# Optimization experiments

Hardware: AMD Instinct MI355X
Metric: run time of the kernel (lower is better)

Reference implementation:

```python
import jax, jax.numpy as jnp
import numpy as np

N_NODES = 100000


def _mean_agg(x, src, dst, n_nodes):
    # gather neighbor (src) features, segment-sum into destination nodes, divide by in-degree
    summed = jax.ops.segment_sum(x[src], dst, num_segments=n_nodes)  # [N, d]
    deg = jax.ops.segment_sum(jnp.ones_like(dst, dtype=x.dtype), dst, num_segments=n_nodes)
    return summed / jnp.clip(deg, 1.0)[:, None]  # DGL clamps zero in-degree to 1


def _sage_conv(x, src, dst, W_self, W_neigh, b, n_nodes):
    h_neigh = _mean_agg(x, src, dst, n_nodes)
    # DGL SAGEConv(mean): fc_self(h_self) + fc_neigh(h_neigh); single bias
    return x @ W_self + h_neigh @ W_neigh + b


def setup_inputs() -> dict:
    key = jax.random.key(0)
    ks = jax.random.split(key, 8)
    in_f, hid_f, out_f = 64, 64, 16
    n_edges = 1200000
    return {
        "x": jax.random.normal(ks[0], (N_NODES, in_f), dtype=jnp.float32),
        "src": jax.random.randint(ks[1], (n_edges,), 0, N_NODES),
        "dst": jax.random.randint(ks[2], (n_edges,), 0, N_NODES),
        "W1_self": jax.random.normal(ks[3], (in_f, hid_f), dtype=jnp.float32) / np.sqrt(in_f),
        "W1_neigh": jax.random.normal(ks[4], (in_f, hid_f), dtype=jnp.float32) / np.sqrt(in_f),
        "b1": jnp.zeros((hid_f,), dtype=jnp.float32),
        "W2_self": jax.random.normal(ks[5], (hid_f, out_f), dtype=jnp.float32) / np.sqrt(hid_f),
        "W2_neigh": jax.random.normal(ks[6], (hid_f, out_f), dtype=jnp.float32) / np.sqrt(hid_f),
        "b2": jnp.zeros((out_f,), dtype=jnp.float32),
    }


def reference(x, src, dst, W1_self, W1_neigh, b1, W2_self, W2_neigh, b2):
    h = _sage_conv(x, src, dst, W1_self, W1_neigh, b1, N_NODES)
    h = jax.nn.relu(h)
    h = _sage_conv(h, src, dst, W2_self, W2_neigh, b2, N_NODES)
    return h
```

## Files before the change

kernel.cpp:

```cpp
#include <hip/hip_runtime.h>

#define N_NODES 100000
#define N_EDGES 1200000
#define BK 128
#define NB 782
#define CHUNK_E 4096
#define NBLK_E 293
#define TOT_H (NB * NBLK_E)
#define NSB2 ((TOT_H + 1023) / 1024)
#define CAP 4096
#define ND1 3125

#define OFF_ROWPTR 0
#define OFF_HISTG  400896
#define OFF_HSCAN  1317632
#define OFF_BLK2   2234368
#define OFF_PAIRS  2235392
#define OFF_SORTED 7035392
#define OFF_Y1     11835392
#define OFF_H1     24635392

__device__ __forceinline__ unsigned short f2bf(float f) {
    unsigned u = __float_as_uint(f);
    unsigned r = (u + 0x7fffu + ((u >> 16) & 1u)) >> 16;
    return (unsigned short)r;
}

__global__ __launch_bounds__(256) void hist_dense1_kernel(
    const int* __restrict__ dst, int* __restrict__ hist_g,
    const float* __restrict__ x,
    const float* __restrict__ Wn, const float* __restrict__ Ws,
    const float* __restrict__ b,
    unsigned short* __restrict__ y1, float* __restrict__ z1)
{
    __shared__ float sx[32 * 64];
    const int t = threadIdx.x;

    if (blockIdx.x < NBLK_E) {
        int* h = (int*)sx;
        const int e0 = blockIdx.x * CHUNK_E;
        const int e1 = min(e0 + CHUNK_E, N_EDGES);
        for (int i = t; i < NB; i += 256) h[i] = 0;
        __syncthreads();
        for (int e = e0 + t; e < e1; e += 256)
            atomicAdd(&h[dst[e] >> 7], 1);
        __syncthreads();
        for (int i = t; i < NB; i += 256)
            hist_g[i * NBLK_E + blockIdx.x] = h[i];
        return;
    }

    const int bid = blockIdx.x - NBLK_E;
    const int w = t >> 6;
    const int lane = t & 63;
    const int half = w >> 1;
    const int nsub = (w & 1) * 16;
    const int chunk = bid * 32;

    {
        const float4* gx = (const float4*)(x + (size_t)chunk * 64);
        float4* sx4 = (float4*)sx;
        sx4[t] = gx[t];
        sx4[t + 256] = gx[t + 256];
    }

    const float* W = half ? Ws : Wn;
    float wr[64];
#pragma unroll
    for (int k = 0; k < 64; ++k) wr[k] = W[k * 64 + lane];
    const float bj = half ? b[lane] : 0.f;

    __syncthreads();

#pragma unroll 1
    for (int m = 0; m < 16; ++m) {
        const int node = nsub + m;
        const float4* xr = (const float4*)(sx + node * 64);
        float a0 = 0.f, a1 = 0.f, a2 = 0.f, a3 = 0.f;
#pragma unroll
        for (int k4 = 0; k4 < 16; ++k4) {
            float4 v = xr[k4];
            a0 += v.x * wr[4 * k4 + 0];
            a1 += v.y * wr[4 * k4 + 1];
            a2 += v.z * wr[4 * k4 + 2];
            a3 += v.w * wr[4 * k4 + 3];
        }
        const float o = (a0 + a1) + (a2 + a3) + bj;
        const size_t gn = (size_t)(chunk + node);
        if (half) z1[gn * 64 + lane] = o;
        else      y1[gn * 64 + lane] = f2bf(o);
    }
}

__global__ __launch_bounds__(1024) void scan2_blocks_kernel(
    const int* __restrict__ hist_g, int* __restrict__ hs_scan, int* __restrict__ blk2)
{
    __shared__ int s[1024];
    int i = blockIdx.x * 1024 + threadIdx.x;
    int v = (i < TOT_H) ? hist_g[i] : 0;
    s[threadIdx.x] = v;
    __syncthreads();
    for (int off = 1; off < 1024; off <<= 1) {
        int t = (threadIdx.x >= off) ? s[threadIdx.x - off] : 0;
        __syncthreads();
        s[threadIdx.x] += t;
        __syncthreads();
    }
    if (i < TOT_H) hs_scan[i] = s[threadIdx.x] - v;
    if (threadIdx.x == 1023) blk2[blockIdx.x] = s[1023];
}

__device__ __forceinline__ void local_tops_scan(const int* blk2, int* tops, int t)
{
    if (t < 256) {
        int v = (t < NSB2) ? blk2[t] : 0;
        tops[t] = v;
    }
    __syncthreads();
    for (int off = 1; off < 256; off <<= 1) {
        int tv = (t >= off && t < 256) ? tops[t - off] : 0;
        __syncthreads();
        if (t < 256) tops[t] += tv;
        __syncthreads();
    }
    int ex = 0;
    if (t < 256) ex = tops[t] - ((t < NSB2) ? blk2[t] : 0);
    __syncthreads();
    if (t < 256) tops[t] = ex;
    __syncthreads();
}

__global__ __launch_bounds__(256) void pair_scatter_kernel(
    const int* __restrict__ src, const int* __restrict__ dst,
    const int* __restrict__ hs_scan, const int* __restrict__ blk2,
    unsigned* __restrict__ pairs)
{
    __shared__ int base_s[NB];
    __shared__ int cur_s[NB];
    __shared__ int tops[256];
    const int b = blockIdx.x;
    const int t = threadIdx.x;
    const int e0 = b * CHUNK_E;
    const int e1 = min(e0 + CHUNK_E, N_EDGES);

    local_tops_scan(blk2, tops, t);

    for (int i = t; i < NB; i += 256) {
        int idx = i * NBLK_E + b;
        base_s[i] = hs_scan[idx] + tops[idx >> 10];
        cur_s[i] = 0;
    }
    __syncthreads();
    for (int e = e0 + t; e < e1; e += 256) {
        int d = dst[e];
        int bk = d >> 7;
        int pos = base_s[bk] + atomicAdd(&cur_s[bk], 1);
        pairs[pos] = ((unsigned)src[e] << 7) | (unsigned)(d & 127);
    }
}

__global__ __launch_bounds__(512) void fused_gather1_kernel(
    const unsigned short* __restrict__ y1,
    const unsigned* __restrict__ pairs,
    const int* __restrict__ hs_scan, const int* __restrict__ blk2,
    int* __restrict__ row_ptr, int* __restrict__ sorted_src,
    float* __restrict__ h1)
{
    __shared__ int slist[CAP];
    __shared__ int hist[BK];
    __shared__ int sc[BK];
    __shared__ int cur[BK];
    __shared__ int tops[256];
    const int b = blockIdx.x;
    const int t = threadIdx.x;
    const int lane = t & 63;
    const int wv = t >> 6;
    const int g = lane >> 3;
    const int fl = lane & 7;

    local_tops_scan(blk2, tops, t);

    const int i0 = b * NBLK_E;
    const int start = hs_scan[i0] + tops[i0 >> 10];
    const int end = (b == NB - 1) ? N_EDGES
                    : hs_scan[i0 + NBLK_E] + tops[(i0 + NBLK_E) >> 10];
    const int cnt = end - start;
    const int node0 = b * BK;

    if (t < BK) hist[t] = 0;
    __syncthreads();
    for (int e = start + t; e < end; e += 512)
        atomicAdd(&hist[pairs[e] & 127u], 1);
    __syncthreads();

    int v = (t < BK) ? hist[t] : 0;
    if (t < BK) sc[t] = v;
    __syncthreads();
    for (int off = 1; off < BK; off <<= 1) {
        int tv = (t >= off && t < BK) ? sc[t - off] : 0;
        __syncthreads();
        if (t < BK) sc[t] += tv;
        __syncthreads();
    }
    const int excl = (t < BK) ? sc[t] - v : 0;
    if (t < BK && node0 + t < N_NODES) row_ptr[node0 + t] = start + excl;
    if (b == NB - 1 && t == 0) row_ptr[N_NODES] = N_EDGES;
    if (t < BK) cur[t] = excl;
    __syncthreads();

    if (cnt <= CAP) {
        for (int e = start + t; e < end; e += 512) {
            unsigned u = pairs[e];
            int p = atomicAdd(&cur[u & 127u], 1);
            slist[p] = (int)(u >> 7);
        }
        __syncthreads();
        for (int i = t; i < cnt; i += 512)
            sorted_src[start + i] = slist[i];
        for (int m = 0; m < 16; ++m) {
            const int node = wv * 16 + m;
            const int gn = node0 + node;
            if (gn >= N_NODES) break;
            const int o = sc[node] - hist[node];
            const int dg = hist[node];
            float a0 = 0.f, a1 = 0.f, a2 = 0.f, a3 = 0.f;
            float a4 = 0.f, a5 = 0.f, a6 = 0.f, a7 = 0.f;
            for (int base = 0; base < dg; base += 8) {
                const int idx = base + g;
                if (idx < dg) {
                    const int s = slist[o + idx];
                    uint4 raw = ((const uint4*)(y1 + (size_t)s * 64))[fl];
                    a0 += __uint_as_float(raw.x << 16);
                    a1 += __uint_as_float(raw.x & 0xffff0000u);
                    a2 += __uint_as_float(raw.y << 16);
                    a3 += __uint_as_float(raw.y & 0xffff0000u);
                    a4 += __uint_as_float(raw.z << 16);
                    a5 += __uint_as_float(raw.z & 0xffff0000u);
                    a6 += __uint_as_float(raw.w << 16);
                    a7 += __uint_as_float(raw.w & 0xffff0000u);
                }
            }
#pragma unroll
            for (int d = 8; d <= 32; d <<= 1) {
                a0 += __shfl_xor(a0, d); a1 += __shfl_xor(a1, d);
                a2 += __shfl_xor(a2, d); a3 += __shfl_xor(a3, d);
                a4 += __shfl_xor(a4, d); a5 += __shfl_xor(a5, d);
                a6 += __shfl_xor(a6, d); a7 += __shfl_xor(a7, d);
            }
            const float invd = 1.0f / (float)max(dg, 1);
            if (g == 0) {
                float4* hp = (float4*)(h1 + (size_t)gn * 64);
                float4 z0 = hp[fl * 2];
                float4 z1v = hp[fl * 2 + 1];
                hp[fl * 2] = make_float4(fmaxf(z0.x + a0 * invd, 0.f),
                                         fmaxf(z0.y + a1 * invd, 0.f),
                                         fmaxf(z0.z + a2 * invd, 0.f),
                                         fmaxf(z0.w + a3 * invd, 0.f));
                hp[fl * 2 + 1] = make_float4(fmaxf(z1v.x + a4 * invd, 0.f),
                                             fmaxf(z1v.y + a5 * invd, 0.f),
                                             fmaxf(z1v.z + a6 * invd, 0.f),
                                             fmaxf(z1v.w + a7 * invd, 0.f));
            }
        }
    } else {
        if (t < BK) cur[t] = start + excl;
        __syncthreads();
        for (int e = start + t; e < end; e += 512) {
            unsigned u = pairs[e];
            int p = atomicAdd(&cur[u & 127u], 1);
            sorted_src[p] = (int)(u >> 7);
        }
        __syncthreads();
        for (int m = 0; m < 16; ++m) {
            const int node = wv * 16 + m;
            const int gn = node0 + node;
            if (gn >= N_NODES) break;
            const int o = start + sc[node] - hist[node];
            const int dg = hist[node];
            float a0 = 0.f, a1 = 0.f, a2 = 0.f, a3 = 0.f;
            float a4 = 0.f, a5 = 0.f, a6 = 0.f, a7 = 0.f;
            for (int base = 0; base < dg; base += 8) {
                const int idx = base + g;
                if (idx < dg) {
                    const int s = sorted_src[o + idx];
                    uint4 raw = ((const uint4*)(y1 + (size_t)s * 64))[fl];
                    a0 += __uint_as_float(raw.x << 16);
                    a1 += __uint_as_float(raw.x & 0xffff0000u);
                    a2 += __uint_as_float(raw.y << 16);
                    a3 += __uint_as_float(raw.y & 0xffff0000u);
                    a4 += __uint_as_float(raw.z << 16);
                    a5 += __uint_as_float(raw.z & 0xffff0000u);
                    a6 += __uint_as_float(raw.w << 16);
                    a7 += __uint_as_float(raw.w & 0xffff0000u);
                }
            }
#pragma unroll
            for (int d = 8; d <= 32; d <<= 1) {
                a0 += __shfl_xor(a0, d); a1 += __shfl_xor(a1, d);
                a2 += __shfl_xor(a2, d); a3 += __shfl_xor(a3, d);
                a4 += __shfl_xor(a4, d); a5 += __shfl_xor(a5, d);
                a6 += __shfl_xor(a6, d); a7 += __shfl_xor(a7, d);
            }
            const float invd = 1.0f / (float)max(dg, 1);
            if (g == 0) {
                float4* hp = (float4*)(h1 + (size_t)gn * 64);
                float4 z0 = hp[fl * 2];
                float4 z1v = hp[fl * 2 + 1];
                hp[fl * 2] = make_float4(fmaxf(z0.x + a0 * invd, 0.f),
                                         fmaxf(z0.y + a1 * invd, 0.f),
                                         fmaxf(z0.z + a2 * invd, 0.f),
                                         fmaxf(z0.w + a3 * invd, 0.f));
                hp[fl * 2 + 1] = make_float4(fmaxf(z1v.x + a4 * invd, 0.f),
                                             fmaxf(z1v.y + a5 * invd, 0.f),
                                             fmaxf(z1v.z + a6 * invd, 0.f),
                                             fmaxf(z1v.w + a7 * invd, 0.f));
            }
        }
    }
}

__global__ __launch_bounds__(256) void dense2_kernel(
    const float* __restrict__ h1,
    const float* __restrict__ Wn, const float* __restrict__ Ws,
    const float* __restrict__ b,
    float* __restrict__ y2, float* __restrict__ out)
{
    __shared__ float sx[32 * 68];
    const int t = threadIdx.x;
    const int w = t >> 6;
    const int lane = t & 63;
    const int half = w >> 1;
    const int nsub = (w & 1) * 16;
    const int j = lane & 15;
    const int g = lane >> 4;
    const int chunk = blockIdx.x * 32;

    {
        const float4* gx = (const float4*)(h1 + (size_t)chunk * 64);
        float4* sx4 = (float4*)sx;
        int r0 = t >> 4, c0 = t & 15;
        sx4[r0 * 17 + c0] = gx[t];
        sx4[(r0 + 16) * 17 + c0] = gx[t + 256];
    }

    const float* W = half ? Ws : Wn;
    float wr[64];
#pragma unroll
    for (int k = 0; k < 64; ++k) wr[k] = W[k * 16 + j];
    const float bj = half ? b[j] : 0.f;

    __syncthreads();

#pragma unroll 1
    for (int q = 0; q < 4; ++q) {
        const int node = nsub + q * 4 + g;
        const float4* xr = (const float4*)(sx + node * 68);
        float a0 = 0.f, a1 = 0.f, a2 = 0.f, a3 = 0.f;
#pragma unroll
        for (int k4 = 0; k4 < 16; ++k4) {
            float4 v = xr[k4];
            a0 += v.x * wr[4 * k4 + 0];
            a1 += v.y * wr[4 * k4 + 1];
            a2 += v.z * wr[4 * k4 + 2];
            a3 += v.w * wr[4 * k4 + 3];
        }
        const float o = (a0 + a1) + (a2 + a3) + bj;
        const size_t gn = (size_t)(chunk + node);
        if (half) out[gn * 16 + j] = o;
        else      y2[gn * 16 + j] = o;
    }
}

__global__ __launch_bounds__(256) void gather2_kernel(
    const float* __restrict__ y2,
    const int* __restrict__ row_ptr,
    const int* __restrict__ sorted_src,
    float* __restrict__ out)
{
    const int wv = threadIdx.x >> 6;
    const int lane = threadIdx.x & 63;
    const int sub = lane >> 4;
    const int sl = lane & 15;
    const int eg = sl >> 2;
    const int fl = sl & 3;

    const int n = blockIdx.x * 16 + wv * 4 + sub;
    const int start = row_ptr[n];
    const int deg = row_ptr[n + 1] - start;

    float4 acc = make_float4(0.f, 0.f, 0.f, 0.f);
    for (int base = 0; base < deg; base += 16) {
        int eid = 0;
        if (base + sl < deg) eid = sorted_src[start + base + sl];
#pragma unroll
        for (int jj = 0; jj < 16; jj += 4) {
            const int idx = jj + eg;
            const int s = __shfl(eid, sub * 16 + idx);
            if (base + idx < deg) {
                float4 v = ((const float4*)(y2 + (size_t)s * 16))[fl];
                acc.x += v.x; acc.y += v.y; acc.z += v.z; acc.w += v.w;
            }
        }
    }
#pragma unroll
    for (int d = 4; d <= 8; d <<= 1) {
        acc.x += __shfl_xor(acc.x, d); acc.y += __shfl_xor(acc.y, d);
        acc.z += __shfl_xor(acc.z, d); acc.w += __shfl_xor(acc.w, d);
    }
    const float invd = 1.0f / (float)max(deg, 1);
    if (eg == 0) {
        float4* op = (float4*)(out + (size_t)n * 16);
        float4 z = op[fl];
        op[fl] = make_float4(z.x + acc.x * invd, z.y + acc.y * invd,
                             z.z + acc.z * invd, z.w + acc.w * invd);
    }
}

extern "C" void kernel_launch(void* const* d_in, const int* in_sizes, int n_in,
                              void* d_out, int out_size, void* d_ws, size_t ws_size,
                              hipStream_t stream) {
    const float* x   = (const float*)d_in[0];
    const int*   src = (const int*)d_in[1];
    const int*   dst = (const int*)d_in[2];
    const float* W1s = (const float*)d_in[3];
    const float* W1n = (const float*)d_in[4];
    const float* b1  = (const float*)d_in[5];
    const float* W2s = (const float*)d_in[6];
    const float* W2n = (const float*)d_in[7];
    const float* b2  = (const float*)d_in[8];
    float* out = (float*)d_out;

    char* ws = (char*)d_ws;
    int* row_ptr    = (int*)(ws + OFF_ROWPTR);
    int* hist_g     = (int*)(ws + OFF_HISTG);
    int* hs_scan    = (int*)(ws + OFF_HSCAN);
    int* blk2       = (int*)(ws + OFF_BLK2);
    unsigned* pairs = (unsigned*)(ws + OFF_PAIRS);
    int* sorted_src = (int*)(ws + OFF_SORTED);
    unsigned short* y1 = (unsigned short*)(ws + OFF_Y1);
    float* y2       = (float*)(ws + OFF_Y1);
    float* h1       = (float*)(ws + OFF_H1);

    hist_dense1_kernel<<<NBLK_E + ND1, 256, 0, stream>>>(
        dst, hist_g, x, W1n, W1s, b1, y1, h1);
    scan2_blocks_kernel<<<NSB2, 1024, 0, stream>>>(hist_g, hs_scan, blk2);
    pair_scatter_kernel<<<NBLK_E, 256, 0, stream>>>(src, dst, hs_scan, blk2, pairs);
    fused_gather1_kernel<<<NB, 512, 0, stream>>>(y1, pairs, hs_scan, blk2,
                                                 row_ptr, sorted_src, h1);
    dense2_kernel<<<ND1, 256, 0, stream>>>(h1, W2n, W2s, b2, y2, out);
    gather2_kernel<<<N_NODES / 16, 256, 0, stream>>>(y2, row_ptr, sorted_src, out);
}
```

Before: 226.7 us.

## Halve bucket size, rework gather1 lane mapping, scan histogram in place

Bucket width drops from 128 to 64 nodes, which doubles the number of gather1 blocks to 1563 and shrinks the shared slist capacity. Gather1 now has each wave handle two nodes at once, with 32 lanes per node and two neighbour loads in flight per iteration. The h1 and out residual values are loaded before the gather loop so their latency overlaps it. The histogram scan is written back into hist_g rather than a separate hs_scan buffer, and the tops scan and pair scatter move to 512 threads. The cost is a larger histogram to scan, more blocks that spill to the global-memory fallback path, and more shuffle and index overhead per node.

```diff
diff --git a/kernel.cpp b/kernel.cpp
--- a/kernel.cpp
+++ b/kernel.cpp
@@ -2,23 +2,22 @@
 
 #define N_NODES 100000
 #define N_EDGES 1200000
-#define BK 128
-#define NB 782
+#define BK 64
+#define NB 1563
 #define CHUNK_E 4096
 #define NBLK_E 293
 #define TOT_H (NB * NBLK_E)
 #define NSB2 ((TOT_H + 1023) / 1024)
-#define CAP 4096
+#define CAP 1536
 #define ND1 3125
 
 #define OFF_ROWPTR 0
-#define OFF_HISTG  400896
-#define OFF_HSCAN  1317632
+#define OFF_HISTG  401408
 #define OFF_BLK2   2234368
-#define OFF_PAIRS  2235392
-#define OFF_SORTED 7035392
-#define OFF_Y1     11835392
-#define OFF_H1     24635392
+#define OFF_PAIRS  2236416
+#define OFF_SORTED 7036928
+#define OFF_Y1     11837440
+#define OFF_H1     24637440
 
 __device__ __forceinline__ unsigned short f2bf(float f) {
     unsigned u = __float_as_uint(f);
@@ -43,7 +42,7 @@
         for (int i = t; i < NB; i += 256) h[i] = 0;
         __syncthreads();
         for (int e = e0 + t; e < e1; e += 256)
-            atomicAdd(&h[dst[e] >> 7], 1);
+            atomicAdd(&h[dst[e] >> 6], 1);
         __syncthreads();
         for (int i = t; i < NB; i += 256)
             hist_g[i * NBLK_E + blockIdx.x] = h[i];
@@ -93,7 +92,7 @@
 }
 
 __global__ __launch_bounds__(1024) void scan2_blocks_kernel(
-    const int* __restrict__ hist_g, int* __restrict__ hs_scan, int* __restrict__ blk2)
+    int* __restrict__ hist_g, int* __restrict__ blk2)
 {
     __shared__ int s[1024];
     int i = blockIdx.x * 1024 + threadIdx.x;
@@ -101,43 +100,40 @@
     s[threadIdx.x] = v;
     __syncthreads();
     for (int off = 1; off < 1024; off <<= 1) {
-        int t = (threadIdx.x >= off) ? s[threadIdx.x - off] : 0;
-        __syncthreads();
-        s[threadIdx.x] += t;
-        __syncthreads();
-    }
-    if (i < TOT_H) hs_scan[i] = s[threadIdx.x] - v;
+        int tv = (threadIdx.x >= off) ? s[threadIdx.x - off] : 0;
+        __syncthreads();
+        s[threadIdx.x] += tv;
+        __syncthreads();
+    }
+    if (i < TOT_H) hist_g[i] = s[threadIdx.x] - v;
     if (threadIdx.x == 1023) blk2[blockIdx.x] = s[1023];
 }
 
 __device__ __forceinline__ void local_tops_scan(const int* blk2, int* tops, int t)
 {
-    if (t < 256) {
-        int v = (t < NSB2) ? blk2[t] : 0;
-        tops[t] = v;
-    }
-    __syncthreads();
-    for (int off = 1; off < 256; off <<= 1) {
-        int tv = (t >= off && t < 256) ? tops[t - off] : 0;
-        __syncthreads();
-        if (t < 256) tops[t] += tv;
-        __syncthreads();
-    }
-    int ex = 0;
-    if (t < 256) ex = tops[t] - ((t < NSB2) ? blk2[t] : 0);
-    __syncthreads();
-    if (t < 256) tops[t] = ex;
-    __syncthreads();
-}
-
-__global__ __launch_bounds__(256) void pair_scatter_kernel(
+    int v = (t < NSB2) ? blk2[t] : 0;
+    tops[t] = v;
+    __syncthreads();
+    for (int off = 1; off < 512; off <<= 1) {
+        int tv = (t >= off) ? tops[t - off] : 0;
+        __syncthreads();
+        tops[t] += tv;
+        __syncthreads();
+    }
+    int ex = tops[t] - v;
+    __syncthreads();
+    tops[t] = ex;
+    __syncthreads();
+}
+
+__global__ __launch_bounds__(512) void pair_scatter_kernel(
     const int* __restrict__ src, const int* __restrict__ dst,
     const int* __restrict__ hs_scan, const int* __restrict__ blk2,
     unsigned* __restrict__ pairs)
 {
     __shared__ int base_s[NB];
     __shared__ int cur_s[NB];
-    __shared__ int tops[256];
+    __shared__ int tops[512];
     const int b = blockIdx.x;
     const int t = threadIdx.x;
     const int e0 = b * CHUNK_E;
@@ -145,17 +141,17 @@
 
     local_tops_scan(blk2, tops, t);
 
-    for (int i = t; i < NB; i += 256) {
+    for (int i = t; i < NB; i += 512) {
         int idx = i * NBLK_E + b;
         base_s[i] = hs_scan[idx] + tops[idx >> 10];
         cur_s[i] = 0;
     }
     __syncthreads();
-    for (int e = e0 + t; e < e1; e += 256) {
+    for (int e = e0 + t; e < e1; e += 512) {
         int d = dst[e];
-        int bk = d >> 7;
+        int bk = d >> 6;
         int pos = base_s[bk] + atomicAdd(&cur_s[bk], 1);
-        pairs[pos] = ((unsigned)src[e] << 7) | (unsigned)(d & 127);
+        pairs[pos] = ((unsigned)src[e] << 6) | (unsigned)(d & 63);
     }
 }
 
@@ -170,13 +166,9 @@
     __shared__ int hist[BK];
     __shared__ int sc[BK];
     __shared__ int cur[BK];
-    __shared__ int tops[256];
+    __shared__ int tops[512];
     const int b = blockIdx.x;
     const int t = threadIdx.x;
-    const int lane = t & 63;
-    const int wv = t >> 6;
-    const int g = lane >> 3;
-    const int fl = lane & 7;
 
     local_tops_scan(blk2, tops, t);
 
@@ -190,7 +182,7 @@
     if (t < BK) hist[t] = 0;
     __syncthreads();
     for (int e = start + t; e < end; e += 512)
-        atomicAdd(&hist[pairs[e] & 127u], 1);
+        atomicAdd(&hist[pairs[e] & 63u], 1);
     __syncthreads();
 
     int v = (t < BK) ? hist[t] : 0;
@@ -208,58 +200,85 @@
     if (t < BK) cur[t] = excl;
     __syncthreads();
 
+    const int wv = t >> 6;
+    const int lane = t & 63;
+    const int sub = lane >> 5;
+    const int sl = lane & 31;
+    const int eg = sl >> 3;
+    const int fl = sl & 7;
+
     if (cnt <= CAP) {
         for (int e = start + t; e < end; e += 512) {
             unsigned u = pairs[e];
-            int p = atomicAdd(&cur[u & 127u], 1);
-            slist[p] = (int)(u >> 7);
+            int p = atomicAdd(&cur[u & 63u], 1);
+            slist[p] = (int)(u >> 6);
         }
         __syncthreads();
         for (int i = t; i < cnt; i += 512)
             sorted_src[start + i] = slist[i];
-        for (int m = 0; m < 16; ++m) {
-            const int node = wv * 16 + m;
+        for (int q = 0; q < 4; ++q) {
+            const int node = wv * 8 + q * 2 + sub;
             const int gn = node0 + node;
             if (gn >= N_NODES) break;
             const int o = sc[node] - hist[node];
             const int dg = hist[node];
+            float4* hp = (float4*)(h1 + (size_t)gn * 64);
+            float4 z;
+            if (eg < 2) z = hp[fl * 2 + eg];
             float a0 = 0.f, a1 = 0.f, a2 = 0.f, a3 = 0.f;
             float a4 = 0.f, a5 = 0.f, a6 = 0.f, a7 = 0.f;
             for (int base = 0; base < dg; base += 8) {
-                const int idx = base + g;
-                if (idx < dg) {
-                    const int s = slist[o + idx];
-                    uint4 raw = ((const uint4*)(y1 + (size_t)s * 64))[fl];
-                    a0 += __uint_as_float(raw.x << 16);
-                    a1 += __uint_as_float(raw.x & 0xffff0000u);
-                    a2 += __uint_as_float(raw.y << 16);
-                    a3 += __uint_as_float(raw.y & 0xffff0000u);
-                    a4 += __uint_as_float(raw.z << 16);
-                    a5 += __uint_as_float(raw.z & 0xffff0000u);
-                    a6 += __uint_as_float(raw.w << 16);
-                    a7 += __uint_as_float(raw.w & 0xffff0000u);
+                const int i0e = base + eg;
+                const int i1e = base + 4 + eg;
+                const bool v0 = i0e < dg, v1 = i1e < dg;
+                uint4 r0, r1;
+                if (v0) {
+                    const int s = slist[o + i0e];
+                    r0 = ((const uint4*)(y1 + (size_t)s * 64))[fl];
                 }
-            }
-#pragma unroll
-            for (int d = 8; d <= 32; d <<= 1) {
+                if (v1) {
+                    const int s = slist[o + i1e];
+                    r1 = ((const uint4*)(y1 + (size_t)s * 64))[fl];
+                }
+                if (v0) {
+                    a0 += __uint_as_float(r0.x << 16);
+                    a1 += __uint_as_float(r0.x & 0xffff0000u);
+                    a2 += __uint_as_float(r0.y << 16);
+                    a3 += __uint_as_float(r0.y & 0xffff0000u);
+                    a4 += __uint_as_float(r0.z << 16);
+                    a5 += __uint_as_float(r0.z & 0xffff0000u);
+                    a6 += __uint_as_float(r0.w << 16);
+                    a7 += __uint_as_float(r0.w & 0xffff0000u);
+                }
+                if (v1) {
+                    a0 += __uint_as_float(r1.x << 16);
+                    a1 += __uint_as_float(r1.x & 0xffff0000u);
+                    a2 += __uint_as_float(r1.y << 16);
+                    a3 += __uint_as_float(r1.y & 0xffff0000u);
+                    a4 += __uint_as_float(r1.z << 16);
+                    a5 += __uint_as_float(r1.z & 0xffff0000u);
+                    a6 += __uint_as_float(r1.w << 16);
+                    a7 += __uint_as_float(r1.w & 0xffff0000u);
+                }
+            }
+#pragma unroll
+            for (int d = 8; d <= 16; d <<= 1) {
                 a0 += __shfl_xor(a0, d); a1 += __shfl_xor(a1, d);
                 a2 += __shfl_xor(a2, d); a3 += __shfl_xor(a3, d);
                 a4 += __shfl_xor(a4, d); a5 += __shfl_xor(a5, d);
                 a6 += __shfl_xor(a6, d); a7 += __shfl_xor(a7, d);
             }
             const float invd = 1.0f / (float)max(dg, 1);
-            if (g == 0) {
-                float4* hp = (float4*)(h1 + (size_t)gn * 64);
-                float4 z0 = hp[fl * 2];
-                float4 z1v = hp[fl * 2 + 1];
-                hp[fl * 2] = make_float4(fmaxf(z0.x + a0 * invd, 0.f),
-                                         fmaxf(z0.y + a1 * invd, 0.f),
-                                         fmaxf(z0.z + a2 * invd, 0.f),
-                                         fmaxf(z0.w + a3 * invd, 0.f));
-                hp[fl * 2 + 1] = make_float4(fmaxf(z1v.x + a4 * invd, 0.f),
-                                             fmaxf(z1v.y + a5 * invd, 0.f),
-                                             fmaxf(z1v.z + a6 * invd, 0.f),
-                                             fmaxf(z1v.w + a7 * invd, 0.f));
+            if (eg == 0) {
+                hp[fl * 2] = make_float4(fmaxf(z.x + a0 * invd, 0.f),
+                                         fmaxf(z.y + a1 * invd, 0.f),
+                                         fmaxf(z.z + a2 * invd, 0.f),
+                                         fmaxf(z.w + a3 * invd, 0.f));
+            } else if (eg == 1) {
+                hp[fl * 2 + 1] = make_float4(fmaxf(z.x + a4 * invd, 0.f),
+                                             fmaxf(z.y + a5 * invd, 0.f),
+                                             fmaxf(z.z + a6 * invd, 0.f),
+                                             fmaxf(z.w + a7 * invd, 0.f));
             }
         }
     } else {
@@ -267,20 +286,23 @@
         __syncthreads();
         for (int e = start + t; e < end; e += 512) {
             unsigned u = pairs[e];
-            int p = atomicAdd(&cur[u & 127u], 1);
-            sorted_src[p] = (int)(u >> 7);
-        }
-        __syncthreads();
-        for (int m = 0; m < 16; ++m) {
-            const int node = wv * 16 + m;
+            int p = atomicAdd(&cur[u & 63u], 1);
+            sorted_src[p] = (int)(u >> 6);
+        }
+        __syncthreads();
+        for (int q = 0; q < 4; ++q) {
+            const int node = wv * 8 + q * 2 + sub;
             const int gn = node0 + node;
             if (gn >= N_NODES) break;
             const int o = start + sc[node] - hist[node];
             const int dg = hist[node];
+            float4* hp = (float4*)(h1 + (size_t)gn * 64);
+            float4 z;
+            if (eg < 2) z = hp[fl * 2 + eg];
             float a0 = 0.f, a1 = 0.f, a2 = 0.f, a3 = 0.f;
             float a4 = 0.f, a5 = 0.f, a6 = 0.f, a7 = 0.f;
-            for (int base = 0; base < dg; base += 8) {
-                const int idx = base + g;
+            for (int base = 0; base < dg; base += 4) {
+                const int idx = base + eg;
                 if (idx < dg) {
                     const int s = sorted_src[o + idx];
                     uint4 raw = ((const uint4*)(y1 + (size_t)s * 64))[fl];
@@ -295,25 +317,23 @@
                 }
             }
 #pragma unroll
-            for (int d = 8; d <= 32; d <<= 1) {
+            for (int d = 8; d <= 16; d <<= 1) {
                 a0 += __shfl_xor(a0, d); a1 += __shfl_xor(a1, d);
                 a2 += __shfl_xor(a2, d); a3 += __shfl_xor(a3, d);
                 a4 += __shfl_xor(a4, d); a5 += __shfl_xor(a5, d);
                 a6 += __shfl_xor(a6, d); a7 += __shfl_xor(a7, d);
             }
             const float invd = 1.0f / (float)max(dg, 1);
-            if (g == 0) {
-                float4* hp = (float4*)(h1 + (size_t)gn * 64);
-                float4 z0 = hp[fl * 2];
-                float4 z1v = hp[fl * 2 + 1];
-                hp[fl * 2] = make_float4(fmaxf(z0.x + a0 * invd, 0.f),
-                                         fmaxf(z0.y + a1 * invd, 0.f),
-                                         fmaxf(z0.z + a2 * invd, 0.f),
-                                         fmaxf(z0.w + a3 * invd, 0.f));
-                hp[fl * 2 + 1] = make_float4(fmaxf(z1v.x + a4 * invd, 0.f),
-                                             fmaxf(z1v.y + a5 * invd, 0.f),
-                                             fmaxf(z1v.z + a6 * invd, 0.f),
-                                             fmaxf(z1v.w + a7 * invd, 0.f));
+            if (eg == 0) {
+                hp[fl * 2] = make_float4(fmaxf(z.x + a0 * invd, 0.f),
+                                         fmaxf(z.y + a1 * invd, 0.f),
+                                         fmaxf(z.z + a2 * invd, 0.f),
+                                         fmaxf(z.w + a3 * invd, 0.f));
+            } else if (eg == 1) {
+                hp[fl * 2 + 1] = make_float4(fmaxf(z.x + a4 * invd, 0.f),
+                                             fmaxf(z.y + a5 * invd, 0.f),
+                                             fmaxf(z.z + a6 * invd, 0.f),
+                                             fmaxf(z.w + a7 * invd, 0.f));
             }
         }
     }
@@ -388,6 +408,10 @@
     const int start = row_ptr[n];
     const int deg = row_ptr[n + 1] - start;
 
+    float4* op = (float4*)(out + (size_t)n * 16);
+    float4 z;
+    if (eg == 0) z = op[fl];
+
     float4 acc = make_float4(0.f, 0.f, 0.f, 0.f);
     for (int base = 0; base < deg; base += 16) {
         int eid = 0;
@@ -409,8 +433,6 @@
     }
     const float invd = 1.0f / (float)max(deg, 1);
     if (eg == 0) {
-        float4* op = (float4*)(out + (size_t)n * 16);
-        float4 z = op[fl];
         op[fl] = make_float4(z.x + acc.x * invd, z.y + acc.y * invd,
                              z.z + acc.z * invd, z.w + acc.w * invd);
     }
@@ -433,7 +455,6 @@
     char* ws = (char*)d_ws;
     int* row_ptr    = (int*)(ws + OFF_ROWPTR);
     int* hist_g     = (int*)(ws + OFF_HISTG);
-    int* hs_scan    = (int*)(ws + OFF_HSCAN);
     int* blk2       = (int*)(ws + OFF_BLK2);
     unsigned* pairs = (unsigned*)(ws + OFF_PAIRS);
     int* sorted_src = (int*)(ws + OFF_SORTED);
@@ -443,9 +464,9 @@
 
     hist_dense1_kernel<<<NBLK_E + ND1, 256, 0, stream>>>(
         dst, hist_g, x, W1n, W1s, b1, y1, h1);
-    scan2_blocks_kernel<<<NSB2, 1024, 0, stream>>>(hist_g, hs_scan, blk2);
-    pair_scatter_kernel<<<NBLK_E, 256, 0, stream>>>(src, dst, hs_scan, blk2, pairs);
-    fused_gather1_kernel<<<NB, 512, 0, stream>>>(y1, pairs, hs_scan, blk2,
+    scan2_blocks_kernel<<<NSB2, 1024, 0, stream>>>(hist_g, blk2);
+    pair_scatter_kernel<<<NBLK_E, 512, 0, stream>>>(src, dst, hist_g, blk2, pairs);
+    fused_gather1_kernel<<<NB, 512, 0, stream>>>(y1, pairs, hist_g, blk2,
                                                  row_ptr, sorted_src, h1);
     dense2_kernel<<<ND1, 256, 0, stream>>>(h1, W2n, W2s, b2, y2, out);
     gather2_kernel<<<N_NODES / 16, 256, 0, stream>>>(y2, row_ptr, sorted_src, out);
```

Result: faster. 219.0 us (-3.4%).
